# Kernel optimization log

Measured on AMD Instinct MI355X. Metric: run time of the kernel, lower is better.

Reference implementation:

```python
import jax, jax.numpy as jnp
import numpy as np

N, E, L, HID, HEADS, G = 50000, 800000, 2, 128, 8, 256
DK = HID // HEADS

def _ln(x, g, b, eps=1e-5):
    m = jnp.mean(x, axis=-1, keepdims=True)
    v = jnp.mean((x - m) ** 2, axis=-1, keepdims=True)
    return (x - m) * jax.lax.rsqrt(v + eps) * g + b

def setup_inputs() -> dict:
    key = jax.random.key(0)
    ks = jax.random.split(key, 24)
    rn = lambda i, s: (0.05 * jax.random.normal(ks[i], s)).astype(jnp.float32)
    return {
        'node_attr': jax.random.randint(ks[0], (N, 4), 0, 64, dtype=jnp.int32),
        'batch_idx': jnp.sort(jax.random.randint(ks[1], (N,), 0, G, dtype=jnp.int32)),
        'edge_index': jax.random.randint(ks[2], (2, E), 0, N, dtype=jnp.int32),
        'strat_dist': jax.random.randint(ks[3], (E,), 0, 32, dtype=jnp.int32),
        'strat_path': jax.random.randint(ks[4], (E,), 0, 16, dtype=jnp.int32),
        'atom_emb': rn(5, (4, 64, HID)),
        'dist_emb': rn(6, (L, 32, HID)),
        'path_emb': rn(7, (L, 16, HID)),
        'Wq': rn(8, (L, HID, HID)), 'bq': rn(9, (L, HID)),
        'Wk': rn(10, (L, HID, HID)), 'bk': rn(11, (L, HID)),
        'Wv': rn(12, (L, HID, HID)), 'bv': rn(13, (L, HID)),
        'Wa': rn(14, (L, HID, HID)), 'ba': rn(15, (L, HID)),
        'ln1_g': jnp.ones((L, HID), jnp.float32), 'ln1_b': jnp.zeros((L, HID), jnp.float32),
        'Wmid': rn(16, (L, HID, 2 * HID)), 'bmid': rn(17, (L, 2 * HID)),
        'Wo': rn(18, (L, 2 * HID, HID)), 'bo': rn(19, (L, HID)),
        'ln2_g': jnp.ones((L, HID), jnp.float32), 'ln2_b': jnp.zeros((L, HID), jnp.float32),
        'W_out': rn(20, (HID, 1)), 'b_out': jnp.zeros((1,), jnp.float32),
    }

def reference(node_attr, batch_idx, edge_index, strat_dist, strat_path,
              atom_emb, dist_emb, path_emb, Wq, bq, Wk, bk, Wv, bv, Wa, ba,
              ln1_g, ln1_b, Wmid, bmid, Wo, bo, ln2_g, ln2_b, W_out, b_out):
    # node encoder: sum of per-feature embeddings (AtomEncoder style)
    x = sum(atom_emb[f][node_attr[:, f]] for f in range(node_attr.shape[1]))  # [N, HID]
    src, tgt = edge_index[0], edge_index[1]  # j (source), i (target)
    inv_sqrt_dk = np.float32(1.0 / np.sqrt(DK))
    for l in range(L):
        # per-edge gather + relational encodings added to the source vector
        s = x[src] + dist_emb[l][strat_dist] + path_emb[l][strat_path]  # [E, HID]
        t = x[tgt]                                                      # [E, HID]
        q = (t @ Wq[l] + bq[l]).reshape(E, HEADS, DK)
        k = (s @ Wk[l] + bk[l]).reshape(E, HEADS, DK)
        v = (s @ Wv[l] + bv[l]).reshape(E, HEADS, DK)
        scores = jnp.sum(q * k, axis=-1) * inv_sqrt_dk  # [E, HEADS]
        # segment softmax keyed on target node id
        smax = jax.ops.segment_max(scores, tgt, num_segments=N)
        ex = jnp.exp(scores - smax[tgt])
        den = jax.ops.segment_sum(ex, tgt, num_segments=N)
        att = ex / (den[tgt] + 1e-16)                   # [E, HEADS]
        msg = (v * att[:, :, None]).reshape(E, HID)
        aggr = jax.ops.segment_sum(msg, tgt, num_segments=N)  # scatter-add
        # update: attn FFN + residual + LayerNorms (dropout is identity in eval)
        h = _ln(jax.nn.gelu(aggr, approximate=False) @ Wa[l] + ba[l] + x, ln1_g[l], ln1_b[l])
        h2 = jax.nn.gelu(h @ Wmid[l] + bmid[l], approximate=False) @ Wo[l] + bo[l]
        x = _ln(h2 + h, ln2_g[l], ln2_b[l])
    # global mean pool per graph, then readout
    cnt = jax.ops.segment_sum(jnp.ones((N,), x.dtype), batch_idx, num_segments=G)
    pooled = jax.ops.segment_sum(x, batch_idx, num_segments=G) / jnp.maximum(cnt, 1.0)[:, None]
    return pooled @ W_out + b_out
```

## Files before the change

kernel.cpp:

```cpp
#include <hip/hip_runtime.h>
#include <hip/hip_bf16.h>
#include <math.h>
#include <stdint.h>

#define N_NODES 50000
#define N_EDGES 800000
#define HID 128
#define NGRAPH 256
#define NLAYER 2
#define CAP 64

#define SCATH 782
#define EHALF 400000

#define CPAD 5

#define ENC_B 3125
#define TKV_B (ENC_B + 1024)
#define RPK_B (TKV_B + 128)
#define PREP_B (RPK_B + 4)

typedef __bf16 bf16x8 __attribute__((ext_vector_type(8)));
typedef __bf16 bf16x2 __attribute__((ext_vector_type(2)));
typedef float f32x4 __attribute__((ext_vector_type(4)));
typedef float f32x2 __attribute__((ext_vector_type(2)));

__device__ __forceinline__ float gelu_f(float v) {
    return 0.5f * v * (1.0f + erff(v * 0.70710678118654752f));
}

__device__ __forceinline__ f32x2 f8lo(uint32_t d) {
    return __builtin_amdgcn_cvt_pk_f32_fp8((int)d, false);
}
__device__ __forceinline__ f32x2 f8hi(uint32_t d) {
    return __builtin_amdgcn_cvt_pk_f32_fp8((int)d, true);
}
__device__ __forceinline__ uint32_t pk4_fp8(float a, float b, float c, float d) {
    int w = __builtin_amdgcn_cvt_pk_fp8_f32(a, b, 0, false);
    w = __builtin_amdgcn_cvt_pk_fp8_f32(c, d, w, true);
    return (uint32_t)w;
}
__device__ __forceinline__ f32x2 bfpair(uint32_t d) {
    f32x2 r;
    r[0] = __uint_as_float(d << 16);
    r[1] = __uint_as_float(d & 0xffff0000u);
    return r;
}

__device__ __forceinline__ void scatter_block(
    int blk, int ebase, int elim,
    const int* __restrict__ tgt, const int* __restrict__ src,
    const int* __restrict__ sd, const int* __restrict__ sp,
    int* __restrict__ cnt, uint32_t* __restrict__ ei) {
    int tid = threadIdx.x;
    int e0 = ebase + blk * 512 + tid;
    int e1 = e0 + 256;
    bool v0 = e0 < elim;
    bool v1 = e1 < elim;
    int t0 = 0, t1 = 0;
    uint32_t p0 = 0, p1 = 0;
    if (v0) {
        t0 = tgt[e0];
        p0 = (uint32_t)src[e0] | ((uint32_t)((sd[e0] << 4) | sp[e0]) << 16);
    }
    if (v1) {
        t1 = tgt[e1];
        p1 = (uint32_t)src[e1] | ((uint32_t)((sd[e1] << 4) | sp[e1]) << 16);
    }
    int r0 = CAP, r1 = CAP;
    if (v0) r0 = atomicAdd(&cnt[t0 << CPAD], 1);
    if (v1) r1 = atomicAdd(&cnt[t1 << CPAD], 1);
    if (v0 && r0 < CAP) ei[(t0 << 6) + r0] = p0;
    if (v1 && r1 < CAP) ei[(t1 << 6) + r1] = p1;
}

__global__ __launch_bounds__(256) void prep_kernel(
    const int* __restrict__ attr, const float* __restrict__ aemb,
    __bf16* __restrict__ xb,
    const float* __restrict__ de, const float* __restrict__ pe,
    const float* __restrict__ Wk, const float* __restrict__ Wv,
    __bf16* __restrict__ tkv,
    const float* __restrict__ Wq, const float* __restrict__ Wa,
    const float* __restrict__ Wmid, const float* __restrict__ Wo,
    __bf16* __restrict__ wqkvf, __bf16* __restrict__ waf,
    __bf16* __restrict__ wmidf, __bf16* __restrict__ wof,
    const int* __restrict__ batch, const float* __restrict__ bout,
    const float* __restrict__ bq, const float* __restrict__ bk,
    const float* __restrict__ bv,
    float* __restrict__ invc, float* __restrict__ outp, float* __restrict__ bqkv,
    const int* __restrict__ tgt, const int* __restrict__ src,
    const int* __restrict__ sd, const int* __restrict__ sp,
    int* __restrict__ cnt, uint32_t* __restrict__ ei) {
    __shared__ float sde[128];
    int b = blockIdx.x;
    int tid = threadIdx.x;
    if (b < SCATH) {
        scatter_block(b, 0, EHALF, tgt, src, sd, sp, cnt, ei);
        return;
    }
    b -= SCATH;
    if (b < ENC_B) {
        int gid = b * 256 + tid;
        int n = gid >> 4;
        int c8 = (gid & 15) << 3;
        const int4 a = *(const int4*)(attr + n * 4);
        const float* r0 = aemb + (size_t)(0 * 64 + a.x) * 128 + c8;
        const float* r1 = aemb + (size_t)(1 * 64 + a.y) * 128 + c8;
        const float* r2 = aemb + (size_t)(2 * 64 + a.z) * 128 + c8;
        const float* r3 = aemb + (size_t)(3 * 64 + a.w) * 128 + c8;
        f32x4 v0a = *(const f32x4*)r0, v0b = *(const f32x4*)(r0 + 4);
        f32x4 v1a = *(const f32x4*)r1, v1b = *(const f32x4*)(r1 + 4);
        f32x4 v2a = *(const f32x4*)r2, v2b = *(const f32x4*)(r2 + 4);
        f32x4 v3a = *(const f32x4*)r3, v3b = *(const f32x4*)(r3 + 4);
        bf16x8 o;
#pragma unroll
        for (int j = 0; j < 4; j++) {
            o[j] = (__bf16)(v0a[j] + v1a[j] + v2a[j] + v3a[j]);
            o[4 + j] = (__bf16)(v0b[j] + v1b[j] + v2b[j] + v3b[j]);
        }
        *(bf16x8*)(xb + (size_t)n * 128 + c8) = o;
    } else if (b < TKV_B) {
        int bb = b - ENC_B;
        int l = bb >> 9;
        int md = bb & 511;
        int dd = md >> 4, pp = md & 15;
        int c = tid;
        if (c < 128) sde[c] = de[l * 4096 + dd * 128 + c] + pe[l * 2048 + pp * 128 + c];
        __syncthreads();
        const float* W = (c < 128) ? (Wk + l * 16384) : (Wv + l * 16384);
        int cc = c & 127;
        float acc = 0.f;
#pragma unroll 4
        for (int k = 0; k < 128; k++) acc = fmaf(sde[k], W[k * 128 + cc], acc);
        tkv[(size_t)bb * 256 + c] = (__bf16)acc;
    } else if (b < RPK_B) {
        int u = (b - TKV_B) * 256 + tid;
        int l = u >> 14, r = u & 16383;
        const float* srcp;
        __bf16* dstp;
        int kg, scol, srcCO;
        if (r < 6144) {
            kg = r / 384;
            int uu = r % 384;
            int sec = uu >> 7, cc = uu & 127;
            scol = ((cc & 15) << 3) | (cc >> 4);
            const float* Ws = (sec == 0) ? Wq : (sec == 1) ? Wk : Wv;
            srcp = Ws + l * 16384;
            srcCO = 128;
            dstp = wqkvf + (size_t)l * 49152 + (size_t)r * 8;
        } else if (r < 8192) {
            int rr = r - 6144;
            kg = rr >> 7;
            int cc = rr & 127;
            scol = ((cc & 15) << 3) | (cc >> 4);
            srcp = Wa + l * 16384;
            srcCO = 128;
            dstp = waf + (size_t)l * 16384 + (size_t)rr * 8;
        } else if (r < 12288) {
            int rr = r - 8192;
            kg = rr >> 8;
            int uu = rr & 255;
            int blk = uu >> 7, cc = uu & 127;
            scol = blk * 128 + (((cc & 15) << 3) | (cc >> 4));
            srcp = Wmid + l * 32768;
            srcCO = 256;
            dstp = wmidf + (size_t)l * 32768 + (size_t)rr * 8;
        } else {
            int rr = r - 12288;
            kg = rr >> 7;
            int cc = rr & 127;
            scol = ((cc & 15) << 3) | (cc >> 4);
            srcp = Wo + l * 32768;
            srcCO = 128;
            dstp = wof + (size_t)l * 32768 + (size_t)rr * 8;
        }
        bf16x8 o;
#pragma unroll
        for (int j = 0; j < 8; j++) o[j] = (__bf16)srcp[(kg * 8 + j) * srcCO + scol];
        *(bf16x8*)dstp = o;
    } else {
        int sb = b - RPK_B;
        if (sb == 0) {
            int g = tid;
            int lo = 0, hi = N_NODES;
            while (lo < hi) { int mid = (lo + hi) >> 1; if (batch[mid] < g) lo = mid + 1; else hi = mid; }
            int start = lo;
            lo = start; hi = N_NODES;
            while (lo < hi) { int mid = (lo + hi) >> 1; if (batch[mid] < g + 1) lo = mid + 1; else hi = mid; }
            int c2 = lo - start;
            invc[g] = 1.0f / fmaxf((float)c2, 1.0f);
            outp[g] = bout[0];
        } else {
            int r = (sb - 1) * 256 + tid;
            int l = r / 384, c = r % 384;
            float v = (c < 128) ? bq[l * 128 + c]
                    : (c < 256) ? bk[l * 128 + c - 128]
                                : bv[l * 128 + c - 256];
            bqkv[r] = v;
        }
    }
}

__global__ __launch_bounds__(256) void qkv_gemm(
    const __bf16* __restrict__ A, const __bf16* __restrict__ Wf,
    const float* __restrict__ bias, __bf16* __restrict__ Qb,
    uint8_t* __restrict__ kv8, int M, int scatN,
    const int* __restrict__ tgt, const int* __restrict__ src,
    const int* __restrict__ sd, const int* __restrict__ sp,
    int* __restrict__ cnt, uint32_t* __restrict__ ei) {
    int tid = threadIdx.x;
    if (blockIdx.x < (unsigned)scatN) {
        scatter_block(blockIdx.x, EHALF, N_EDGES, tgt, src, sd, sp, cnt, ei);
        return;
    }
    int bq = blockIdx.x - scatN;
    int sec = bq % 3;
    int rowblk = bq / 3;
    int lane = tid & 63;
    int wv = tid >> 6;
    int row0 = rowblk * 64 + wv * 16;
    int col0 = sec * 128;
    if (row0 >= M) return;
    int quad = lane >> 4, tq = lane & 15;
    f32x4 acc[8] = {};
#pragma unroll
    for (int k0 = 0; k0 < 128; k0 += 32) {
        int rr = row0 + tq;
        if (rr >= M) rr = M - 1;
        bf16x8 af = *(const bf16x8*)(A + (size_t)rr * 128 + k0 + quad * 8);
#pragma unroll
        for (int nt = 0; nt < 8; nt++) {
            bf16x8 bfr = *(const bf16x8*)(Wf + ((size_t)((k0 >> 3) + quad) * 384 + col0 + nt * 16 + tq) * 8);
            acc[nt] = __builtin_amdgcn_mfma_f32_16x16x32_bf16(af, bfr, acc[nt], 0, 0, 0);
        }
    }
    int cb = tq * 8;
    float bia[8];
#pragma unroll
    for (int t = 0; t < 8; t++) bia[t] = bias[col0 + cb + t];
#pragma unroll
    for (int v = 0; v < 4; v++) {
        int rr = row0 + quad * 4 + v;
        if (rr >= M) continue;
        float val[8];
#pragma unroll
        for (int t = 0; t < 8; t++) val[t] = acc[t][v] + bia[t];
        if (sec == 0) {
            bf16x8 ov;
#pragma unroll
            for (int t = 0; t < 8; t++) ov[t] = (__bf16)val[t];
            *(bf16x8*)(Qb + (size_t)rr * 128 + cb) = ov;
        } else {
            uint2 st;
            st.x = pk4_fp8(val[0], val[1], val[2], val[3]);
            st.y = pk4_fp8(val[4], val[5], val[6], val[7]);
            *(uint2*)(kv8 + (size_t)rr * 256 + (sec - 1) * 128 + cb) = st;
        }
    }
}

template <int CI, bool GOUT, bool LN, bool POOL>
__global__ __launch_bounds__(256) void mfma_gemm(
    const __bf16* __restrict__ A, const __bf16* __restrict__ Wf,
    const float* __restrict__ bias, const __bf16* __restrict__ res,
    const float* __restrict__ lng, const float* __restrict__ lnb,
    __bf16* outb,
    const int* __restrict__ batch, const float* __restrict__ invc,
    const float* __restrict__ WoutV, float* __restrict__ outp,
    int M, int CO) {
    __shared__ float ps[POOL ? NGRAPH : 1];
    int lane = threadIdx.x & 63;
    int wv = threadIdx.x >> 6;
    int row0 = blockIdx.y * 64 + wv * 16;
    int col0 = blockIdx.x * 128;
    bool active = row0 < M;
    if (POOL) {
        ps[threadIdx.x] = 0.f;
        __syncthreads();
    } else if (!active) {
        return;
    }
    int quad = lane >> 4, tq = lane & 15;
    if (active) {
        f32x4 acc[8] = {};
#pragma unroll
        for (int k0 = 0; k0 < CI; k0 += 32) {
            int rr = row0 + tq;
            if (rr >= M) rr = M - 1;
            bf16x8 af = *(const bf16x8*)(A + (size_t)rr * CI + k0 + quad * 8);
#pragma unroll
            for (int nt = 0; nt < 8; nt++) {
                bf16x8 bfr = *(const bf16x8*)(Wf + ((size_t)((k0 >> 3) + quad) * CO + col0 + nt * 16 + tq) * 8);
                acc[nt] = __builtin_amdgcn_mfma_f32_16x16x32_bf16(af, bfr, acc[nt], 0, 0, 0);
            }
        }
        int cb = col0 + tq * 8;
        float bia[8] = {};
        if (bias) {
#pragma unroll
            for (int t = 0; t < 8; t++) bia[t] = bias[cb + t];
        }
        float gv[8], bv2[8];
        if (LN) {
#pragma unroll
            for (int t = 0; t < 8; t++) { gv[t] = lng[cb + t]; bv2[t] = lnb[cb + t]; }
        }
        float wo8[8];
        if (POOL) {
#pragma unroll
            for (int t = 0; t < 8; t++) wo8[t] = WoutV[cb + t];
        }
#pragma unroll
        for (int v = 0; v < 4; v++) {
            int rr = row0 + quad * 4 + v;
            if (rr >= M) continue;
            float val[8];
#pragma unroll
            for (int nt = 0; nt < 8; nt++) val[nt] = acc[nt][v] + bia[nt];
            if (res) {
                bf16x8 rv = *(const bf16x8*)(res + (size_t)rr * 128 + tq * 8);
#pragma unroll
                for (int t = 0; t < 8; t++) val[t] += (float)rv[t];
            }
            if (GOUT) {
#pragma unroll
                for (int t = 0; t < 8; t++) val[t] = gelu_f(val[t]);
            }
            if (LN) {
                float s = 0.f, s2 = 0.f;
#pragma unroll
                for (int t = 0; t < 8; t++) { s += val[t]; s2 = fmaf(val[t], val[t], s2); }
#pragma unroll
                for (int o = 1; o < 16; o <<= 1) {
                    s += __shfl_xor(s, o);
                    s2 += __shfl_xor(s2, o);
                }
                float m = s * (1.0f / 128.0f);
                float var = s2 * (1.0f / 128.0f) - m * m;
                float rs = rsqrtf(var + 1e-5f);
#pragma unroll
                for (int t = 0; t < 8; t++) val[t] = (val[t] - m) * rs * gv[t] + bv2[t];
            }
            if (outb) {
                bf16x8 ov;
#pragma unroll
                for (int t = 0; t < 8; t++) ov[t] = (__bf16)val[t];
                *(bf16x8*)(outb + (size_t)rr * CO + cb) = ov;
            }
            if (POOL) {
                float dot = 0.f;
#pragma unroll
                for (int t = 0; t < 8; t++) dot = fmaf(val[t], wo8[t], dot);
#pragma unroll
                for (int o = 1; o < 16; o <<= 1) dot += __shfl_xor(dot, o);
                if (tq == 0) {
                    int g = batch[rr];
                    atomicAdd(&ps[g], dot * invc[g]);
                }
            }
        }
    }
    if (POOL) {
        __syncthreads();
        float pv = ps[threadIdx.x];
        if (pv != 0.f) atomicAdd(&outp[threadIdx.x], pv);
    }
}

__global__ __launch_bounds__(256) void attn_kernel(
    const __bf16* __restrict__ Qb, const uint8_t* __restrict__ kv8,
    const __bf16* __restrict__ tkv,
    const int* __restrict__ cnt, const uint32_t* __restrict__ ei,
    __bf16* __restrict__ outb) {
    __shared__ float red[4][1376];
    int wv = threadIdx.x >> 6;
    int i = blockIdx.x * 4 + wv;
    int lane = threadIdx.x & 63;
    int slot = lane >> 3, h = lane & 7;
    int ch0 = h * 16;
    const uint4* qv = (const uint4*)(Qb + (size_t)i * 128 + ch0);
    uint4 qa = qv[0], qb = qv[1];
    uint32_t qd[8] = {qa.x, qa.y, qa.z, qa.w, qb.x, qb.y, qb.z, qb.w};
    f32x2 qp[8];
#pragma unroll
    for (int j = 0; j < 8; j++) qp[j] = bfpair(qd[j]);
    int deg = cnt[i << CPAD];
    if (deg > CAP) deg = CAP;
    int p0 = i << 6;
    int p1 = p0 + deg;
    float l = 0.f;
    f32x2 ap[8] = {};
    int p = p0 + slot;
    uint32_t w1 = 0, w2 = 0;
    if (p < p1) w1 = ei[p];
    if (p + 8 < p1) w2 = ei[p + 8];
    uint4 kw, vw, t0, t1, u0, u1;
    {
        int j = w1 & 0xffff, md = w1 >> 16;
        const uint8_t* kr = kv8 + (size_t)j * 256 + ch0;
        kw = *(const uint4*)kr;
        vw = *(const uint4*)(kr + 128);
        const __bf16* tr = tkv + md * 256 + ch0;
        t0 = *(const uint4*)tr;
        t1 = *(const uint4*)(tr + 8);
        u0 = *(const uint4*)(tr + 128);
        u1 = *(const uint4*)(tr + 136);
    }
    while (p < p1) {
        uint4 kwn, vwn, t0n, t1n, u0n, u1n;
        {
            int j = w2 & 0xffff, md = w2 >> 16;
            const uint8_t* kr = kv8 + (size_t)j * 256 + ch0;
            kwn = *(const uint4*)kr;
            vwn = *(const uint4*)(kr + 128);
            const __bf16* tr = tkv + md * 256 + ch0;
            t0n = *(const uint4*)tr;
            t1n = *(const uint4*)(tr + 8);
            u0n = *(const uint4*)(tr + 128);
            u1n = *(const uint4*)(tr + 136);
        }
        uint32_t w3 = w2;
        if (p + 16 < p1) w3 = ei[p + 16];
        uint32_t kd[4] = {kw.x, kw.y, kw.z, kw.w};
        uint32_t vd[4] = {vw.x, vw.y, vw.z, vw.w};
        uint32_t td[8] = {t0.x, t0.y, t0.z, t0.w, t1.x, t1.y, t1.z, t1.w};
        uint32_t ud[8] = {u0.x, u0.y, u0.z, u0.w, u1.x, u1.y, u1.z, u1.w};
        f32x2 sa = {0.f, 0.f};
#pragma unroll
        for (int j = 0; j < 4; j++) {
            f32x2 klo = f8lo(kd[j]) + bfpair(td[2 * j]);
            f32x2 khi = f8hi(kd[j]) + bfpair(td[2 * j + 1]);
            sa = qp[2 * j] * klo + sa;
            sa = qp[2 * j + 1] * khi + sa;
        }
        float s = sa[0] + sa[1];
        float pe = __expf(s * 0.25f);
        l += pe;
        f32x2 pp = {pe, pe};
#pragma unroll
        for (int j = 0; j < 4; j++) {
            f32x2 vlo = f8lo(vd[j]) + bfpair(ud[2 * j]);
            f32x2 vhi = f8hi(vd[j]) + bfpair(ud[2 * j + 1]);
            ap[2 * j] = pp * vlo + ap[2 * j];
            ap[2 * j + 1] = pp * vhi + ap[2 * j + 1];
        }
        kw = kwn; vw = vwn; t0 = t0n; t1 = t1n; u0 = u0n; u1 = u1n;
        w2 = w3;
        p += 8;
    }
    float* rw = red[wv] + slot * 172 + 20 * h;
#pragma unroll
    for (int j = 0; j < 8; j++) *(f32x2*)(rw + 2 * j) = ap[j];
    red[wv][slot * 172 + 156 + h] = l;
    asm volatile("" ::: "memory");
    int pc = 2 * lane + 4 * (lane >> 3);
    int hh = lane >> 3;
    float s0 = 0.f, s1 = 0.f, ls = 0.f;
#pragma unroll
    for (int s = 0; s < 8; s++) {
        float2 v = *(const float2*)(red[wv] + s * 172 + pc);
        s0 += v.x;
        s1 += v.y;
        ls += red[wv][s * 172 + 156 + hh];
    }
    float inv = 1.0f / (ls + 1e-16f);
    bf16x2 o2;
    o2[0] = (__bf16)gelu_f(s0 * inv);
    o2[1] = (__bf16)gelu_f(s1 * inv);
    *(bf16x2*)(outb + (size_t)i * 128 + 2 * lane) = o2;
}

extern "C" void kernel_launch(void* const* d_in, const int* in_sizes, int n_in,
                              void* d_out, int out_size, void* d_ws, size_t ws_size,
                              hipStream_t stream) {
    const int N = N_NODES, E = N_EDGES;
    const int* node_attr = (const int*)d_in[0];
    const int* batch_idx = (const int*)d_in[1];
    const int* edge_index = (const int*)d_in[2];
    const int* strat_dist = (const int*)d_in[3];
    const int* strat_path = (const int*)d_in[4];
    const float* atom_emb = (const float*)d_in[5];
    const float* dist_emb = (const float*)d_in[6];
    const float* path_emb = (const float*)d_in[7];
    const float* Wq = (const float*)d_in[8];
    const float* bq = (const float*)d_in[9];
    const float* Wk = (const float*)d_in[10];
    const float* bk = (const float*)d_in[11];
    const float* Wv = (const float*)d_in[12];
    const float* bv = (const float*)d_in[13];
    const float* Wa = (const float*)d_in[14];
    const float* ba = (const float*)d_in[15];
    const float* ln1g = (const float*)d_in[16];
    const float* ln1b = (const float*)d_in[17];
    const float* Wmid = (const float*)d_in[18];
    const float* bmid = (const float*)d_in[19];
    const float* Wo = (const float*)d_in[20];
    const float* bo = (const float*)d_in[21];
    const float* ln2g = (const float*)d_in[22];
    const float* ln2b = (const float*)d_in[23];
    const float* Wout = (const float*)d_in[24];
    const float* bout = (const float*)d_in[25];
    float* out = (float*)d_out;

    const int* src = edge_index;
    const int* tgt = edge_index + E;

    size_t NF = (size_t)N * HID;
    float* invc = (float*)d_ws;
    float* bqkv = invc + 256;
    __bf16* xb = (__bf16*)(bqkv + 768);
    __bf16* Qb = xb + NF;
    __bf16* ab = Qb + NF;
    __bf16* midb = ab + NF;
    __bf16* tkv = midb + 2 * NF;
    __bf16* wqkvf = tkv + 262144;
    __bf16* waf = wqkvf + 98304;
    __bf16* wmidf = waf + 32768;
    __bf16* wof = wmidf + 65536;
    uint8_t* kv8 = (uint8_t*)(wof + 65536);
    uint32_t* ei = (uint32_t*)(kv8 + (size_t)N * 256);
    int* cnt = (int*)(ei + (size_t)N * CAP);

    hipMemsetAsync(cnt, 0, (size_t)N * 32 * sizeof(int), stream);
    prep_kernel<<<SCATH + PREP_B, 256, 0, stream>>>(
        node_attr, atom_emb, xb,
        dist_emb, path_emb, Wk, Wv, tkv,
        Wq, Wa, Wmid, Wo, wqkvf, waf, wmidf, wof,
        batch_idx, bout, bq, bk, bv, invc, out, bqkv,
        tgt, src, strat_dist, strat_path, cnt, ei);

    const int GB = (N + 63) / 64;
    const int AB = (N + 3) / 4;

    for (int l = 0; l < NLAYER; ++l) {
        int scatN = (l == 0) ? SCATH : 0;
        qkv_gemm<<<scatN + 3 * GB, 256, 0, stream>>>(
            xb, wqkvf + l * 49152, bqkv + l * 384, Qb, kv8, N, scatN,
            tgt, src, strat_dist, strat_path, cnt, ei);

        attn_kernel<<<AB, 256, 0, stream>>>(Qb, kv8, tkv + l * 131072, cnt, ei, ab);

        mfma_gemm<128, false, true, false><<<dim3(1, GB), 256, 0, stream>>>(
            ab, waf + l * 16384, ba + l * 128, xb, ln1g + l * 128, ln1b + l * 128,
            ab, nullptr, nullptr, nullptr, nullptr, N, 128);
        mfma_gemm<128, true, false, false><<<dim3(2, GB), 256, 0, stream>>>(
            ab, wmidf + l * 32768, bmid + l * 256, nullptr, nullptr, nullptr,
            midb, nullptr, nullptr, nullptr, nullptr, N, 256);
        if (l < NLAYER - 1) {
            mfma_gemm<256, false, true, false><<<dim3(1, GB), 256, 0, stream>>>(
                midb, wof + l * 32768, bo + l * 128, ab, ln2g + l * 128, ln2b + l * 128,
                xb, nullptr, nullptr, nullptr, nullptr, N, 128);
        } else {
            mfma_gemm<256, false, true, true><<<dim3(1, GB), 256, 0, stream>>>(
                midb, wof + l * 32768, bo + l * 128, ab, ln2g + l * 128, ln2b + l * 128,
                nullptr, batch_idx, invc, Wout, out, N, 128);
        }
    }
}
```

Before: 421.0 us.

## Fuse FFN mid and output GEMMs via LDS; remap attention to 8 lanes per node

Adds an ffn_fused kernel that computes the 128->256 GELU projection into shared memory per 16-row wave tile, then immediately applies the 256->128 projection with residual, LayerNorm and optional pooling. This removes the midb intermediate round trip through global memory and one kernel launch per layer. Separately, attention is restructured so that each node is handled by 8 lanes, one per head, walking its edges sequentially and reducing scores with shuffles. This replaces the previous 64-lane per-node layout with its shared-memory cross-slot reduction, but it lowers memory-level parallelism per node and serialises high-degree nodes.

```diff
diff --git a/kernel.cpp b/kernel.cpp
--- a/kernel.cpp
+++ b/kernel.cpp
@@ -367,33 +367,153 @@
     }
 }
 
-__global__ __launch_bounds__(256) void attn_kernel(
+template <bool POOL>
+__global__ __launch_bounds__(256) void ffn_fused(
+    const __bf16* __restrict__ A,
+    const __bf16* __restrict__ Wmf,
+    const float* __restrict__ bmid,
+    const __bf16* __restrict__ Wof,
+    const float* __restrict__ bo,
+    const float* __restrict__ lng, const float* __restrict__ lnb,
+    __bf16* outb,
+    const int* __restrict__ batch, const float* __restrict__ invc,
+    const float* __restrict__ WoutV, float* __restrict__ outp,
+    int M) {
+    __shared__ __bf16 smid[4][16][264];
+    __shared__ float ps[POOL ? NGRAPH : 1];
+    int lane = threadIdx.x & 63;
+    int wv = threadIdx.x >> 6;
+    int row0 = blockIdx.x * 64 + wv * 16;
+    bool active = row0 < M;
+    if (POOL) {
+        ps[threadIdx.x] = 0.f;
+        __syncthreads();
+    } else if (!active) {
+        return;
+    }
+    int quad = lane >> 4, tq = lane & 15;
+    if (active) {
+#pragma unroll
+        for (int cH = 0; cH < 2; ++cH) {
+            f32x4 acc[8] = {};
+#pragma unroll
+            for (int k0 = 0; k0 < 128; k0 += 32) {
+                int rr = row0 + tq;
+                if (rr >= M) rr = M - 1;
+                bf16x8 af = *(const bf16x8*)(A + (size_t)rr * 128 + k0 + quad * 8);
+#pragma unroll
+                for (int nt = 0; nt < 8; nt++) {
+                    bf16x8 bfr = *(const bf16x8*)(Wmf + ((size_t)((k0 >> 3) + quad) * 256 + cH * 128 + nt * 16 + tq) * 8);
+                    acc[nt] = __builtin_amdgcn_mfma_f32_16x16x32_bf16(af, bfr, acc[nt], 0, 0, 0);
+                }
+            }
+            int cb = cH * 128 + tq * 8;
+            float bia[8];
+#pragma unroll
+            for (int t = 0; t < 8; t++) bia[t] = bmid[cb + t];
+#pragma unroll
+            for (int v = 0; v < 4; v++) {
+                int lr = quad * 4 + v;
+                bf16x8 ov;
+#pragma unroll
+                for (int t = 0; t < 8; t++) ov[t] = (__bf16)gelu_f(acc[t][v] + bia[t]);
+                *(bf16x8*)(&smid[wv][lr][cb]) = ov;
+            }
+        }
+        asm volatile("" ::: "memory");
+        f32x4 acc[8] = {};
+#pragma unroll
+        for (int k0 = 0; k0 < 256; k0 += 32) {
+            bf16x8 af = *(const bf16x8*)(&smid[wv][tq][k0 + quad * 8]);
+#pragma unroll
+            for (int nt = 0; nt < 8; nt++) {
+                bf16x8 bfr = *(const bf16x8*)(Wof + ((size_t)((k0 >> 3) + quad) * 128 + nt * 16 + tq) * 8);
+                acc[nt] = __builtin_amdgcn_mfma_f32_16x16x32_bf16(af, bfr, acc[nt], 0, 0, 0);
+            }
+        }
+        int cb = tq * 8;
+        float bia[8], gv[8], bv2[8], wo8[8];
+#pragma unroll
+        for (int t = 0; t < 8; t++) {
+            bia[t] = bo[cb + t];
+            gv[t] = lng[cb + t];
+            bv2[t] = lnb[cb + t];
+        }
+        if (POOL) {
+#pragma unroll
+            for (int t = 0; t < 8; t++) wo8[t] = WoutV[cb + t];
+        }
+#pragma unroll
+        for (int v = 0; v < 4; v++) {
+            int rr = row0 + quad * 4 + v;
+            if (rr >= M) continue;
+            float val[8];
+            bf16x8 rv = *(const bf16x8*)(A + (size_t)rr * 128 + cb);
+#pragma unroll
+            for (int t = 0; t < 8; t++) val[t] = acc[t][v] + bia[t] + (float)rv[t];
+            float s = 0.f, s2 = 0.f;
+#pragma unroll
+            for (int t = 0; t < 8; t++) { s += val[t]; s2 = fmaf(val[t], val[t], s2); }
+#pragma unroll
+            for (int o = 1; o < 16; o <<= 1) {
+                s += __shfl_xor(s, o);
+                s2 += __shfl_xor(s2, o);
+            }
+            float m = s * (1.0f / 128.0f);
+            float var = s2 * (1.0f / 128.0f) - m * m;
+            float rs = rsqrtf(var + 1e-5f);
+#pragma unroll
+            for (int t = 0; t < 8; t++) val[t] = (val[t] - m) * rs * gv[t] + bv2[t];
+            if (!POOL) {
+                bf16x8 ov;
+#pragma unroll
+                for (int t = 0; t < 8; t++) ov[t] = (__bf16)val[t];
+                *(bf16x8*)(outb + (size_t)rr * 128 + cb) = ov;
+            } else {
+                float dot = 0.f;
+#pragma unroll
+                for (int t = 0; t < 8; t++) dot = fmaf(val[t], wo8[t], dot);
+#pragma unroll
+                for (int o = 1; o < 16; o <<= 1) dot += __shfl_xor(dot, o);
+                if (tq == 0) {
+                    int g = batch[rr];
+                    atomicAdd(&ps[g], dot * invc[g]);
+                }
+            }
+        }
+    }
+    if (POOL) {
+        __syncthreads();
+        float pv = ps[threadIdx.x];
+        if (pv != 0.f) atomicAdd(&outp[threadIdx.x], pv);
+    }
+}
+
+__global__ __launch_bounds__(512) void attn_kernel(
     const __bf16* __restrict__ Qb, const uint8_t* __restrict__ kv8,
     const __bf16* __restrict__ tkv,
     const int* __restrict__ cnt, const uint32_t* __restrict__ ei,
     __bf16* __restrict__ outb) {
-    __shared__ float red[4][1376];
-    int wv = threadIdx.x >> 6;
-    int i = blockIdx.x * 4 + wv;
-    int lane = threadIdx.x & 63;
-    int slot = lane >> 3, h = lane & 7;
+    int i = blockIdx.x * 64 + (threadIdx.x >> 3);
+    int h = threadIdx.x & 7;
     int ch0 = h * 16;
-    const uint4* qv = (const uint4*)(Qb + (size_t)i * 128 + ch0);
+    int iq = (i < N_NODES) ? i : N_NODES - 1;
+    const uint4* qv = (const uint4*)(Qb + (size_t)iq * 128 + ch0);
     uint4 qa = qv[0], qb = qv[1];
     uint32_t qd[8] = {qa.x, qa.y, qa.z, qa.w, qb.x, qb.y, qb.z, qb.w};
     f32x2 qp[8];
 #pragma unroll
     for (int j = 0; j < 8; j++) qp[j] = bfpair(qd[j]);
-    int deg = cnt[i << CPAD];
+    int deg = (i < N_NODES) ? cnt[i << CPAD] : 0;
     if (deg > CAP) deg = CAP;
-    int p0 = i << 6;
+    int p0 = iq << 6;
     int p1 = p0 + deg;
     float l = 0.f;
     f32x2 ap[8] = {};
-    int p = p0 + slot;
+    int p = p0;
     uint32_t w1 = 0, w2 = 0;
     if (p < p1) w1 = ei[p];
-    if (p + 8 < p1) w2 = ei[p + 8];
+    if (p + 1 < p1) w2 = ei[p + 1];
     uint4 kw, vw, t0, t1, u0, u1;
     {
         int j = w1 & 0xffff, md = w1 >> 16;
@@ -420,7 +540,7 @@
             u1n = *(const uint4*)(tr + 136);
         }
         uint32_t w3 = w2;
-        if (p + 16 < p1) w3 = ei[p + 16];
+        if (p + 2 < p1) w3 = ei[p + 2];
         uint32_t kd[4] = {kw.x, kw.y, kw.z, kw.w};
         uint32_t vd[4] = {vw.x, vw.y, vw.z, vw.w};
         uint32_t td[8] = {t0.x, t0.y, t0.z, t0.w, t1.x, t1.y, t1.z, t1.w};
@@ -434,6 +554,9 @@
             sa = qp[2 * j + 1] * khi + sa;
         }
         float s = sa[0] + sa[1];
+        s += __shfl_xor(s, 1);
+        s += __shfl_xor(s, 2);
+        s += __shfl_xor(s, 4);
         float pe = __expf(s * 0.25f);
         l += pe;
         f32x2 pp = {pe, pe};
@@ -446,28 +569,21 @@
         }
         kw = kwn; vw = vwn; t0 = t0n; t1 = t1n; u0 = u0n; u1 = u1n;
         w2 = w3;
-        p += 8;
-    }
-    float* rw = red[wv] + slot * 172 + 20 * h;
-#pragma unroll
-    for (int j = 0; j < 8; j++) *(f32x2*)(rw + 2 * j) = ap[j];
-    red[wv][slot * 172 + 156 + h] = l;
-    asm volatile("" ::: "memory");
-    int pc = 2 * lane + 4 * (lane >> 3);
-    int hh = lane >> 3;
-    float s0 = 0.f, s1 = 0.f, ls = 0.f;
-#pragma unroll
-    for (int s = 0; s < 8; s++) {
-        float2 v = *(const float2*)(red[wv] + s * 172 + pc);
-        s0 += v.x;
-        s1 += v.y;
-        ls += red[wv][s * 172 + 156 + hh];
-    }
-    float inv = 1.0f / (ls + 1e-16f);
-    bf16x2 o2;
-    o2[0] = (__bf16)gelu_f(s0 * inv);
-    o2[1] = (__bf16)gelu_f(s1 * inv);
-    *(bf16x2*)(outb + (size_t)i * 128 + 2 * lane) = o2;
+        p += 1;
+    }
+    if (i >= N_NODES) return;
+    float inv = 1.0f / (l + 1e-16f);
+    bf16x8 o1, o2;
+#pragma unroll
+    for (int j = 0; j < 4; j++) {
+        o1[2 * j] = (__bf16)gelu_f(ap[j][0] * inv);
+        o1[2 * j + 1] = (__bf16)gelu_f(ap[j][1] * inv);
+        o2[2 * j] = (__bf16)gelu_f(ap[4 + j][0] * inv);
+        o2[2 * j + 1] = (__bf16)gelu_f(ap[4 + j][1] * inv);
+    }
+    __bf16* op = outb + (size_t)i * 128 + ch0;
+    *(bf16x8*)op = o1;
+    *(bf16x8*)(op + 8) = o2;
 }
 
 extern "C" void kernel_launch(void* const* d_in, const int* in_sizes, int n_in,
@@ -511,8 +627,7 @@
     __bf16* xb = (__bf16*)(bqkv + 768);
     __bf16* Qb = xb + NF;
     __bf16* ab = Qb + NF;
-    __bf16* midb = ab + NF;
-    __bf16* tkv = midb + 2 * NF;
+    __bf16* tkv = ab + NF;
     __bf16* wqkvf = tkv + 262144;
     __bf16* waf = wqkvf + 98304;
     __bf16* wmidf = waf + 32768;
@@ -530,7 +645,7 @@
         tgt, src, strat_dist, strat_path, cnt, ei);
 
     const int GB = (N + 63) / 64;
-    const int AB = (N + 3) / 4;
+    const int AB = (N + 63) / 64;
 
     for (int l = 0; l < NLAYER; ++l) {
         int scatN = (l == 0) ? SCATH : 0;
@@ -538,22 +653,21 @@
             xb, wqkvf + l * 49152, bqkv + l * 384, Qb, kv8, N, scatN,
             tgt, src, strat_dist, strat_path, cnt, ei);
 
-        attn_kernel<<<AB, 256, 0, stream>>>(Qb, kv8, tkv + l * 131072, cnt, ei, ab);
+        attn_kernel<<<AB, 512, 0, stream>>>(Qb, kv8, tkv + l * 131072, cnt, ei, ab);
 
         mfma_gemm<128, false, true, false><<<dim3(1, GB), 256, 0, stream>>>(
             ab, waf + l * 16384, ba + l * 128, xb, ln1g + l * 128, ln1b + l * 128,
             ab, nullptr, nullptr, nullptr, nullptr, N, 128);
-        mfma_gemm<128, true, false, false><<<dim3(2, GB), 256, 0, stream>>>(
-            ab, wmidf + l * 32768, bmid + l * 256, nullptr, nullptr, nullptr,
-            midb, nullptr, nullptr, nullptr, nullptr, N, 256);
         if (l < NLAYER - 1) {
-            mfma_gemm<256, false, true, false><<<dim3(1, GB), 256, 0, stream>>>(
-                midb, wof + l * 32768, bo + l * 128, ab, ln2g + l * 128, ln2b + l * 128,
-                xb, nullptr, nullptr, nullptr, nullptr, N, 128);
+            ffn_fused<false><<<GB, 256, 0, stream>>>(
+                ab, wmidf + l * 32768, bmid + l * 256, wof + l * 32768, bo + l * 128,
+                ln2g + l * 128, ln2b + l * 128, xb,
+                nullptr, nullptr, nullptr, nullptr, N);
         } else {
-            mfma_gemm<256, false, true, true><<<dim3(1, GB), 256, 0, stream>>>(
-                midb, wof + l * 32768, bo + l * 128, ab, ln2g + l * 128, ln2b + l * 128,
-                nullptr, batch_idx, invc, Wout, out, N, 128);
-        }
-    }
-}
+            ffn_fused<true><<<GB, 256, 0, stream>>>(
+                ab, wmidf + l * 32768, bmid + l * 256, wof + l * 32768, bo + l * 128,
+                ln2g + l * 128, ln2b + l * 128, nullptr,
+                batch_idx, invc, Wout, out, N);
+        }
+    }
+}
```

Measured after the change: 429.5 us. 1.02x slower.

## Fuse attention-out, FFN mid and output GEMMs into one per-row kernel

Applied to the files above, without the earlier changes.

Replaces three separate MFMA GEMM launches per layer (Wa+LN1, Wmid+GELU, Wo+LN2/pool) with a single kernel. Each wave keeps its 16-row intermediate activations (h and the 256-wide mid) in LDS. This removes the global round trips for the h and mid buffers (the mid buffer is dropped from the workspace) and two launches per layer. In exchange it uses more LDS per block, which can lower occupancy, and each wave runs three GEMMs serially.

```diff
diff --git a/kernel.cpp b/kernel.cpp
--- a/kernel.cpp
+++ b/kernel.cpp
@@ -259,20 +259,25 @@
     }
 }
 
-template <int CI, bool GOUT, bool LN, bool POOL>
-__global__ __launch_bounds__(256) void mfma_gemm(
-    const __bf16* __restrict__ A, const __bf16* __restrict__ Wf,
-    const float* __restrict__ bias, const __bf16* __restrict__ res,
-    const float* __restrict__ lng, const float* __restrict__ lnb,
-    __bf16* outb,
+template <bool POOL>
+__global__ __launch_bounds__(256) void ffn_uber(
+    const __bf16* __restrict__ A,
+    const __bf16* __restrict__ xres,
+    const __bf16* __restrict__ Waf, const float* __restrict__ ba,
+    const float* __restrict__ l1g, const float* __restrict__ l1b,
+    const __bf16* __restrict__ Wmf, const float* __restrict__ bmid,
+    const __bf16* __restrict__ Wof, const float* __restrict__ bo,
+    const float* __restrict__ l2g, const float* __restrict__ l2b,
+    __bf16* __restrict__ outx,
     const int* __restrict__ batch, const float* __restrict__ invc,
     const float* __restrict__ WoutV, float* __restrict__ outp,
-    int M, int CO) {
+    int M) {
+    __shared__ __bf16 hld[4][16][136];
+    __shared__ __bf16 smid[4][16][264];
     __shared__ float ps[POOL ? NGRAPH : 1];
     int lane = threadIdx.x & 63;
     int wv = threadIdx.x >> 6;
-    int row0 = blockIdx.y * 64 + wv * 16;
-    int col0 = blockIdx.x * 128;
+    int row0 = blockIdx.x * 64 + wv * 16;
     bool active = row0 < M;
     if (POOL) {
         ps[threadIdx.x] = 0.f;
@@ -282,51 +287,35 @@
     }
     int quad = lane >> 4, tq = lane & 15;
     if (active) {
-        f32x4 acc[8] = {};
-#pragma unroll
-        for (int k0 = 0; k0 < CI; k0 += 32) {
-            int rr = row0 + tq;
-            if (rr >= M) rr = M - 1;
-            bf16x8 af = *(const bf16x8*)(A + (size_t)rr * CI + k0 + quad * 8);
-#pragma unroll
-            for (int nt = 0; nt < 8; nt++) {
-                bf16x8 bfr = *(const bf16x8*)(Wf + ((size_t)((k0 >> 3) + quad) * CO + col0 + nt * 16 + tq) * 8);
-                acc[nt] = __builtin_amdgcn_mfma_f32_16x16x32_bf16(af, bfr, acc[nt], 0, 0, 0);
-            }
-        }
-        int cb = col0 + tq * 8;
-        float bia[8] = {};
-        if (bias) {
-#pragma unroll
-            for (int t = 0; t < 8; t++) bia[t] = bias[cb + t];
-        }
-        float gv[8], bv2[8];
-        if (LN) {
-#pragma unroll
-            for (int t = 0; t < 8; t++) { gv[t] = lng[cb + t]; bv2[t] = lnb[cb + t]; }
-        }
-        float wo8[8];
-        if (POOL) {
-#pragma unroll
-            for (int t = 0; t < 8; t++) wo8[t] = WoutV[cb + t];
-        }
-#pragma unroll
-        for (int v = 0; v < 4; v++) {
-            int rr = row0 + quad * 4 + v;
-            if (rr >= M) continue;
-            float val[8];
-#pragma unroll
-            for (int nt = 0; nt < 8; nt++) val[nt] = acc[nt][v] + bia[nt];
-            if (res) {
-                bf16x8 rv = *(const bf16x8*)(res + (size_t)rr * 128 + tq * 8);
-#pragma unroll
-                for (int t = 0; t < 8; t++) val[t] += (float)rv[t];
-            }
-            if (GOUT) {
-#pragma unroll
-                for (int t = 0; t < 8; t++) val[t] = gelu_f(val[t]);
-            }
-            if (LN) {
+        int cb = tq * 8;
+        {
+            f32x4 acc[8] = {};
+#pragma unroll
+            for (int k0 = 0; k0 < 128; k0 += 32) {
+                int rr = row0 + tq;
+                if (rr >= M) rr = M - 1;
+                bf16x8 af = *(const bf16x8*)(A + (size_t)rr * 128 + k0 + quad * 8);
+#pragma unroll
+                for (int nt = 0; nt < 8; nt++) {
+                    bf16x8 bfr = *(const bf16x8*)(Waf + ((size_t)((k0 >> 3) + quad) * 128 + nt * 16 + tq) * 8);
+                    acc[nt] = __builtin_amdgcn_mfma_f32_16x16x32_bf16(af, bfr, acc[nt], 0, 0, 0);
+                }
+            }
+            float bia[8], gv[8], bv2[8];
+#pragma unroll
+            for (int t = 0; t < 8; t++) {
+                bia[t] = ba[cb + t];
+                gv[t] = l1g[cb + t];
+                bv2[t] = l1b[cb + t];
+            }
+#pragma unroll
+            for (int v = 0; v < 4; v++) {
+                int rr = row0 + quad * 4 + v;
+                int rc = (rr < M) ? rr : M - 1;
+                bf16x8 rv = *(const bf16x8*)(xres + (size_t)rc * 128 + cb);
+                float val[8];
+#pragma unroll
+                for (int t = 0; t < 8; t++) val[t] = acc[t][v] + bia[t] + (float)rv[t];
                 float s = 0.f, s2 = 0.f;
 #pragma unroll
                 for (int t = 0; t < 8; t++) { s += val[t]; s2 = fmaf(val[t], val[t], s2); }
@@ -338,16 +327,86 @@
                 float m = s * (1.0f / 128.0f);
                 float var = s2 * (1.0f / 128.0f) - m * m;
                 float rs = rsqrtf(var + 1e-5f);
-#pragma unroll
-                for (int t = 0; t < 8; t++) val[t] = (val[t] - m) * rs * gv[t] + bv2[t];
-            }
-            if (outb) {
                 bf16x8 ov;
 #pragma unroll
+                for (int t = 0; t < 8; t++) ov[t] = (__bf16)((val[t] - m) * rs * gv[t] + bv2[t]);
+                *(bf16x8*)(&hld[wv][quad * 4 + v][cb]) = ov;
+            }
+        }
+        asm volatile("" ::: "memory");
+#pragma unroll
+        for (int cH = 0; cH < 2; ++cH) {
+            f32x4 acc[8] = {};
+#pragma unroll
+            for (int k0 = 0; k0 < 128; k0 += 32) {
+                bf16x8 af = *(const bf16x8*)(&hld[wv][tq][k0 + quad * 8]);
+#pragma unroll
+                for (int nt = 0; nt < 8; nt++) {
+                    bf16x8 bfr = *(const bf16x8*)(Wmf + ((size_t)((k0 >> 3) + quad) * 256 + cH * 128 + nt * 16 + tq) * 8);
+                    acc[nt] = __builtin_amdgcn_mfma_f32_16x16x32_bf16(af, bfr, acc[nt], 0, 0, 0);
+                }
+            }
+            int cb2 = cH * 128 + cb;
+            float bia[8];
+#pragma unroll
+            for (int t = 0; t < 8; t++) bia[t] = bmid[cb2 + t];
+#pragma unroll
+            for (int v = 0; v < 4; v++) {
+                bf16x8 ov;
+#pragma unroll
+                for (int t = 0; t < 8; t++) ov[t] = (__bf16)gelu_f(acc[t][v] + bia[t]);
+                *(bf16x8*)(&smid[wv][quad * 4 + v][cb2]) = ov;
+            }
+        }
+        asm volatile("" ::: "memory");
+        f32x4 acc[8] = {};
+#pragma unroll
+        for (int k0 = 0; k0 < 256; k0 += 32) {
+            bf16x8 af = *(const bf16x8*)(&smid[wv][tq][k0 + quad * 8]);
+#pragma unroll
+            for (int nt = 0; nt < 8; nt++) {
+                bf16x8 bfr = *(const bf16x8*)(Wof + ((size_t)((k0 >> 3) + quad) * 128 + nt * 16 + tq) * 8);
+                acc[nt] = __builtin_amdgcn_mfma_f32_16x16x32_bf16(af, bfr, acc[nt], 0, 0, 0);
+            }
+        }
+        float bia[8], gv[8], bv2[8], wo8[8];
+#pragma unroll
+        for (int t = 0; t < 8; t++) {
+            bia[t] = bo[cb + t];
+            gv[t] = l2g[cb + t];
+            bv2[t] = l2b[cb + t];
+        }
+        if (POOL) {
+#pragma unroll
+            for (int t = 0; t < 8; t++) wo8[t] = WoutV[cb + t];
+        }
+#pragma unroll
+        for (int v = 0; v < 4; v++) {
+            int rr = row0 + quad * 4 + v;
+            bf16x8 rv = *(const bf16x8*)(&hld[wv][quad * 4 + v][cb]);
+            float val[8];
+#pragma unroll
+            for (int t = 0; t < 8; t++) val[t] = acc[t][v] + bia[t] + (float)rv[t];
+            float s = 0.f, s2 = 0.f;
+#pragma unroll
+            for (int t = 0; t < 8; t++) { s += val[t]; s2 = fmaf(val[t], val[t], s2); }
+#pragma unroll
+            for (int o = 1; o < 16; o <<= 1) {
+                s += __shfl_xor(s, o);
+                s2 += __shfl_xor(s2, o);
+            }
+            float m = s * (1.0f / 128.0f);
+            float var = s2 * (1.0f / 128.0f) - m * m;
+            float rs = rsqrtf(var + 1e-5f);
+#pragma unroll
+            for (int t = 0; t < 8; t++) val[t] = (val[t] - m) * rs * gv[t] + bv2[t];
+            if (rr >= M) continue;
+            if (!POOL) {
+                bf16x8 ov;
+#pragma unroll
                 for (int t = 0; t < 8; t++) ov[t] = (__bf16)val[t];
-                *(bf16x8*)(outb + (size_t)rr * CO + cb) = ov;
-            }
-            if (POOL) {
+                *(bf16x8*)(outx + (size_t)rr * 128 + cb) = ov;
+            } else {
                 float dot = 0.f;
 #pragma unroll
                 for (int t = 0; t < 8; t++) dot = fmaf(val[t], wo8[t], dot);
@@ -511,8 +570,7 @@
     __bf16* xb = (__bf16*)(bqkv + 768);
     __bf16* Qb = xb + NF;
     __bf16* ab = Qb + NF;
-    __bf16* midb = ab + NF;
-    __bf16* tkv = midb + 2 * NF;
+    __bf16* tkv = ab + NF;
     __bf16* wqkvf = tkv + 262144;
     __bf16* waf = wqkvf + 98304;
     __bf16* wmidf = waf + 32768;
@@ -540,20 +598,18 @@
 
         attn_kernel<<<AB, 256, 0, stream>>>(Qb, kv8, tkv + l * 131072, cnt, ei, ab);
 
-        mfma_gemm<128, false, true, false><<<dim3(1, GB), 256, 0, stream>>>(
-            ab, waf + l * 16384, ba + l * 128, xb, ln1g + l * 128, ln1b + l * 128,
-            ab, nullptr, nullptr, nullptr, nullptr, N, 128);
-        mfma_gemm<128, true, false, false><<<dim3(2, GB), 256, 0, stream>>>(
-            ab, wmidf + l * 32768, bmid + l * 256, nullptr, nullptr, nullptr,
-            midb, nullptr, nullptr, nullptr, nullptr, N, 256);
         if (l < NLAYER - 1) {
-            mfma_gemm<256, false, true, false><<<dim3(1, GB), 256, 0, stream>>>(
-                midb, wof + l * 32768, bo + l * 128, ab, ln2g + l * 128, ln2b + l * 128,
-                xb, nullptr, nullptr, nullptr, nullptr, N, 128);
+            ffn_uber<false><<<GB, 256, 0, stream>>>(
+                ab, xb, waf + l * 16384, ba + l * 128, ln1g + l * 128, ln1b + l * 128,
+                wmidf + l * 32768, bmid + l * 256, wof + l * 32768, bo + l * 128,
+                ln2g + l * 128, ln2b + l * 128, xb,
+                nullptr, nullptr, nullptr, nullptr, N);
         } else {
-            mfma_gemm<256, false, true, true><<<dim3(1, GB), 256, 0, stream>>>(
-                midb, wof + l * 32768, bo + l * 128, ab, ln2g + l * 128, ln2b + l * 128,
-                nullptr, batch_idx, invc, Wout, out, N, 128);
-        }
-    }
-}
+            ffn_uber<true><<<GB, 256, 0, stream>>>(
+                ab, xb, waf + l * 16384, ba + l * 128, ln1g + l * 128, ln1b + l * 128,
+                wmidf + l * 32768, bmid + l * 256, wof + l * 32768, bo + l * 128,
+                ln2g + l * 128, ln2b + l * 128, nullptr,
+                batch_idx, invc, Wout, out, N);
+        }
+    }
+}
```

New measurement: 380.1 us. 1.11x faster.
